# Kernel tuning notes

Measured on AMD Instinct MI355X. Metric: run time of the kernel, lower is better.

Reference implementation:

```python
import jax, jax.numpy as jnp
import numpy as np

N_NODES = 100000
EMB_DIM = 128
N_LAYERS = 3
N_EDGES = 1600000


def setup_inputs() -> dict:
    key = jax.random.key(0)
    ks = jax.random.split(key, 6)
    edge_index = jax.random.randint(ks[0], (2, N_EDGES), 0, N_NODES, dtype=jnp.int32)
    deg_inv = jax.random.uniform(ks[1], (N_NODES,), dtype=jnp.float32)
    node_emb = 0.02 * jax.random.normal(ks[2], (N_NODES, EMB_DIM), dtype=jnp.float32)
    W = jax.random.normal(ks[3], (N_LAYERS, EMB_DIM, EMB_DIM), dtype=jnp.float32) / np.sqrt(EMB_DIM)
    b = jnp.zeros((N_LAYERS, EMB_DIM), dtype=jnp.float32)
    gamma = jnp.ones((EMB_DIM,), dtype=jnp.float32)
    beta = jnp.zeros((EMB_DIM,), dtype=jnp.float32)
    return {"edge_index": edge_index, "deg_inv": deg_inv, "node_emb": node_emb,
            "W": W, "b": b, "gamma": gamma, "beta": beta}


def reference(edge_index, deg_inv, node_emb, W, b, gamma, beta):
    src, dst = edge_index[0], edge_index[1]
    x = node_emb  # [N, d]
    for l in range(N_LAYERS):
        # scatter-add neighbor aggregation: m[v] = sum_{(u->v)} x[u]
        m = jax.ops.segment_sum(x[src], dst, num_segments=N_NODES)  # [N, d]
        m = m * deg_inv[:, None]
        h = jax.nn.gelu(m @ W[l] + b[l], approximate=False)  # dropout=0 (eval)
        x = x + h  # residual
    # LayerNorm over feature dim
    mu = jnp.mean(x, axis=-1, keepdims=True)
    var = jnp.var(x, axis=-1, keepdims=True)
    x = (x - mu) * jax.lax.rsqrt(var + 1e-5) * gamma + beta
    return x
```

## Files before the change

kernel.cpp:

```cpp
#include <hip/hip_runtime.h>
#include <hip/hip_bf16.h>
#include <math.h>

#define N_NODES 100000
#define EMB 128
#define N_EDGES 1600000
#define N_LAYERS 3

#define NB 400
#define NPB 250
#define CAP 8192
#define CAPB 6144
#define BSTR 16
#define EPT 8
#define BUCKET_THREADS 512
#define BUCKET_BLOCKS ((N_EDGES + BUCKET_THREADS * EPT - 1) / (BUCKET_THREADS * EPT))

typedef __bf16 bf16x8 __attribute__((ext_vector_type(8)));
typedef float f32x4 __attribute__((ext_vector_type(4)));


__global__ __launch_bounds__(BUCKET_THREADS) void bucket_kernel(
    const int* __restrict__ src, const int* __restrict__ dst,
    int* __restrict__ bcur, unsigned* __restrict__ pairs) {
  __shared__ int scnt[NB];
  __shared__ int sbase[NB];
  const int t = threadIdx.x;
  if (t < NB) scnt[t] = 0;
  __syncthreads();
  unsigned pk[EPT];
  int bk[EPT], lofs[EPT];
  const int base_e = blockIdx.x * BUCKET_THREADS * EPT;
#pragma unroll
  for (int it = 0; it < EPT; ++it) {
    int i = base_e + it * BUCKET_THREADS + t;
    bk[it] = -1;
    if (i < N_EDGES) {
      int d = dst[i];
      int s = src[i];
      int b = d / NPB;
      int vloc = d - b * NPB;
      bk[it] = b;
      pk[it] = ((unsigned)vloc << 17) | (unsigned)s;
      lofs[it] = atomicAdd(&scnt[b], 1);
    }
  }
  __syncthreads();
  if (t < NB) sbase[t] = atomicAdd(&bcur[t * BSTR], scnt[t]);
  __syncthreads();
#pragma unroll
  for (int it = 0; it < EPT; ++it) {
    if (bk[it] >= 0) {
      int idx = sbase[bk[it]] + lofs[it];
      if (idx < CAP) pairs[(size_t)bk[it] * CAP + idx] = pk[it];
    }
  }
}

__device__ __forceinline__ int* scan512(int* pin, int* pout, int t) {
  for (int off = 1; off < 512; off <<= 1) {
    for (int i = t; i < 512; i += 256) {
      int v = pin[i];
      if (i >= off) v += pin[i - off];
      pout[i] = v;
    }
    __syncthreads();
    int* tmp = pin; pin = pout; pout = tmp;
  }
  return pin;
}

__global__ __launch_bounds__(256) void fillb_kernel(const unsigned* __restrict__ pairs,
                                                    const int* __restrict__ bcur,
                                                    int* __restrict__ row_ptr,
                                                    int* __restrict__ col) {
  __shared__ int sA[512], sB[512];
  __shared__ int cnt[NPB], cur[NPB];
  __shared__ unsigned pstage[CAPB];
  __shared__ int colstage[CAPB];
  const int t = threadIdx.x;
  const int b = blockIdx.x;

  for (int i = t; i < 512; i += 256) sA[i] = (i < NB) ? bcur[i * BSTR] : 0;
  __syncthreads();
  int* r = scan512(sA, sB, t);
  int base_b = b ? r[b - 1] : 0;
  int n = r[b] - base_b;
  if (n > CAP) n = CAP;
  const unsigned* pg = pairs + (size_t)b * CAP;
  const bool fits = (n <= CAPB);

  if (fits) for (int i = t; i < n; i += 256) pstage[i] = pg[i];
  if (t < NPB) cnt[t] = 0;
  __syncthreads();
  for (int i = t; i < n; i += 256) atomicAdd(&cnt[(fits ? pstage[i] : pg[i]) >> 17], 1);
  __syncthreads();
  for (int i = t; i < 512; i += 256) sA[i] = (i < NPB) ? cnt[i] : 0;
  __syncthreads();
  r = scan512(sA, sB, t);
  if (t < NPB) {
    int ex = r[t] - cnt[t];
    row_ptr[b * NPB + t] = base_b + ex;
    cur[t] = ex;
  }
  if (b == NB - 1 && t == 0) row_ptr[N_NODES] = N_EDGES;
  __syncthreads();
  for (int i = t; i < n; i += 256) {
    unsigned p = fits ? pstage[i] : pg[i];
    int pos = atomicAdd(&cur[p >> 17], 1);
    int s = (int)(p & 0x1FFFFu);
    if (fits) colstage[pos] = s;
    else col[base_b + pos] = s;
  }
  __syncthreads();
  if (fits) for (int i = t; i < n; i += 256) col[base_b + i] = colstage[i];
}


__global__ __launch_bounds__(256) void tobf16_kernel(const float* __restrict__ in,
                                                     __hip_bfloat16* __restrict__ xb) {
  size_t i = (size_t)blockIdx.x * 256 + threadIdx.x;
  const float4* p = (const float4*)in + i * 2;
  float4 a = p[0], b = p[1];
  union { __hip_bfloat16 h[8]; uint4 u; } r;
  r.h[0] = __float2bfloat16(a.x); r.h[1] = __float2bfloat16(a.y);
  r.h[2] = __float2bfloat16(a.z); r.h[3] = __float2bfloat16(a.w);
  r.h[4] = __float2bfloat16(b.x); r.h[5] = __float2bfloat16(b.y);
  r.h[6] = __float2bfloat16(b.z); r.h[7] = __float2bfloat16(b.w);
  ((uint4*)xb)[i] = r.u;
}

__global__ __launch_bounds__(256) void wt_kernel(const float* __restrict__ W,
                                                 __hip_bfloat16* __restrict__ WT) {
  int l = blockIdx.x;
  const float* Wl = W + (size_t)l * EMB * EMB;
  __hip_bfloat16* WTl = WT + (size_t)l * EMB * EMB;
  for (int i = threadIdx.x; i < EMB * EMB; i += 256) {
    int k = i >> 7, c = i & 127;
    WTl[c * EMB + k] = __float2bfloat16(Wl[i]);
  }
}


__device__ __forceinline__ float bf_lo(unsigned int w) { return __uint_as_float(w << 16); }
__device__ __forceinline__ float bf_hi(unsigned int w) { return __uint_as_float(w & 0xFFFF0000u); }

__device__ __forceinline__ float gelu_exact(float v) {
  return 0.5f * v * (1.f + erff(v * 0.70710678118654752f));
}

template <int LAST>
__global__ __launch_bounds__(256, LAST ? 5 : 8) void fused_kernel(
    const __hip_bfloat16* __restrict__ xb_in,
    const int* __restrict__ row_ptr,
    const int* __restrict__ col,
    const float* __restrict__ deg_inv,
    const __hip_bfloat16* __restrict__ WTl,
    const float* __restrict__ bias,
    __hip_bfloat16* __restrict__ xb_out,
    float* __restrict__ xf_out,
    const float* __restrict__ gamma,
    const float* __restrict__ beta) {
  __shared__ __hip_bfloat16 sM[32][136];
  __shared__ float sX[LAST ? 32 * 129 : 1];

  const int t = threadIdx.x;
  const int w = t >> 6;
  const int lane = t & 63;
  const int q = lane >> 4;
  const int l15 = lane & 15;
  const int row0b = blockIdx.x * 32;

  const char* gbase = (const char*)xb_in + l15 * 16;
  for (int nn = 0; nn < 8; ++nn) {
    const int v = __builtin_amdgcn_readfirstlane(row0b + w * 8 + nn);
    const int beg = row_ptr[v], end = row_ptr[v + 1];
    float a0 = 0.f, a1 = 0.f, a2 = 0.f, a3 = 0.f, a4 = 0.f, a5 = 0.f, a6 = 0.f, a7 = 0.f;
#define ACC8(W) { a0 += bf_lo(W.x); a1 += bf_hi(W.x); a2 += bf_lo(W.y); a3 += bf_hi(W.y); \
                  a4 += bf_lo(W.z); a5 += bf_hi(W.z); a6 += bf_lo(W.w); a7 += bf_hi(W.w); }
    int e = beg;
    for (; e + 16 <= end; e += 16) {
      int u0 = col[e + q];
      int u1 = col[e + 4 + q];
      int u2 = col[e + 8 + q];
      int u3 = col[e + 12 + q];
      uint4 w0 = *(const uint4*)(gbase + (size_t)u0 * 256);
      uint4 w1 = *(const uint4*)(gbase + (size_t)u1 * 256);
      uint4 w2 = *(const uint4*)(gbase + (size_t)u2 * 256);
      uint4 w3 = *(const uint4*)(gbase + (size_t)u3 * 256);
      ACC8(w0) ACC8(w1) ACC8(w2) ACC8(w3)
    }
    for (; e < end; e += 4) {
      int idx = e + q;
      bool valid = idx < end;
      int u = col[valid ? idx : beg];
      uint4 w0 = *(const uint4*)(gbase + (size_t)u * 256);
      if (valid) ACC8(w0)
    }
#undef ACC8
    a0 += __shfl_xor(a0, 16, 64); a0 += __shfl_xor(a0, 32, 64);
    a1 += __shfl_xor(a1, 16, 64); a1 += __shfl_xor(a1, 32, 64);
    a2 += __shfl_xor(a2, 16, 64); a2 += __shfl_xor(a2, 32, 64);
    a3 += __shfl_xor(a3, 16, 64); a3 += __shfl_xor(a3, 32, 64);
    a4 += __shfl_xor(a4, 16, 64); a4 += __shfl_xor(a4, 32, 64);
    a5 += __shfl_xor(a5, 16, 64); a5 += __shfl_xor(a5, 32, 64);
    a6 += __shfl_xor(a6, 16, 64); a6 += __shfl_xor(a6, 32, 64);
    a7 += __shfl_xor(a7, 16, 64); a7 += __shfl_xor(a7, 32, 64);
    if (q == 0) {
      float di = deg_inv[v];
      union { __hip_bfloat16 h[8]; uint4 u4; } r;
      r.h[0] = __float2bfloat16(a0 * di); r.h[1] = __float2bfloat16(a1 * di);
      r.h[2] = __float2bfloat16(a2 * di); r.h[3] = __float2bfloat16(a3 * di);
      r.h[4] = __float2bfloat16(a4 * di); r.h[5] = __float2bfloat16(a5 * di);
      r.h[6] = __float2bfloat16(a6 * di); r.h[7] = __float2bfloat16(a7 * di);
      *(uint4*)(&sM[w * 8 + nn][l15 * 8]) = r.u4;
    }
  }

  const int rh = w >> 1, ch = w & 1;
  const int lhi = q;
  bf16x8 bfr[4][4];
#pragma unroll
  for (int ct = 0; ct < 4; ++ct) {
    const __hip_bfloat16* wp = WTl + (size_t)(ch * 64 + ct * 16 + l15) * EMB + lhi * 8;
#pragma unroll
    for (int ks = 0; ks < 4; ++ks)
      bfr[ct][ks] = *(const bf16x8*)(wp + ks * 32);
  }
  __syncthreads();

  f32x4 acc[4];
#pragma unroll
  for (int ct = 0; ct < 4; ++ct) acc[ct] = (f32x4)(0.f);
#pragma unroll
  for (int ks = 0; ks < 4; ++ks) {
    bf16x8 af = *(const bf16x8*)(&sM[rh * 16 + l15][lhi * 8 + ks * 32]);
#pragma unroll
    for (int ct = 0; ct < 4; ++ct)
      acc[ct] = __builtin_amdgcn_mfma_f32_16x16x32_bf16(af, bfr[ct][ks], acc[ct], 0, 0, 0);
  }

#pragma unroll
  for (int ct = 0; ct < 4; ++ct) {
    const int colg = ch * 64 + ct * 16 + l15;
    const float bb = bias[colg];
#pragma unroll
    for (int j = 0; j < 4; ++j) {
      const int rloc = rh * 16 + lhi * 4 + j;
      const size_t off = (size_t)(row0b + rloc) * EMB + colg;
      float xv = __bfloat162float(xb_in[off]) + gelu_exact(acc[ct][j] + bb);
      if (!LAST) xb_out[off] = __float2bfloat16(xv);
      else sX[rloc * 129 + colg] = xv;
    }
  }

  if (LAST) {
    __syncthreads();
    float g1 = gamma[lane], g2 = gamma[lane + 64];
    float b1 = beta[lane], b2 = beta[lane + 64];
    for (int rr = 0; rr < 8; ++rr) {
      int r = w * 8 + rr;
      float v1 = sX[r * 129 + lane], v2 = sX[r * 129 + lane + 64];
      float s = v1 + v2;
      float sq = fmaf(v1, v1, v2 * v2);
      for (int off = 1; off < 64; off <<= 1) {
        s += __shfl_xor(s, off, 64);
        sq += __shfl_xor(sq, off, 64);
      }
      float mu = s * (1.f / EMB);
      float var = sq * (1.f / EMB) - mu * mu;
      float rstd = rsqrtf(var + 1e-5f);
      size_t rowoff = (size_t)(row0b + r) * EMB;
      xf_out[rowoff + lane] = (v1 - mu) * rstd * g1 + b1;
      xf_out[rowoff + lane + 64] = (v2 - mu) * rstd * g2 + b2;
    }
  }
}


extern "C" void kernel_launch(void* const* d_in, const int* in_sizes, int n_in,
                              void* d_out, int out_size, void* d_ws, size_t ws_size,
                              hipStream_t stream) {
  const int* edge_index = (const int*)d_in[0];
  const float* deg_inv = (const float*)d_in[1];
  const float* node_emb = (const float*)d_in[2];
  const float* W = (const float*)d_in[3];
  const float* b = (const float*)d_in[4];
  const float* gamma = (const float*)d_in[5];
  const float* beta = (const float*)d_in[6];
  const int* src = edge_index;
  const int* dst = edge_index + N_EDGES;
  float* x = (float*)d_out;

  char* ws = (char*)d_ws;
  auto take = [&](size_t bytes) {
    char* p = ws;
    ws += (bytes + 255) & ~(size_t)255;
    return p;
  };
  __hip_bfloat16* xbA = (__hip_bfloat16*)take((size_t)N_NODES * EMB * 2);
  __hip_bfloat16* xbB = (__hip_bfloat16*)take((size_t)N_NODES * EMB * 2);
  __hip_bfloat16* WT = (__hip_bfloat16*)take((size_t)N_LAYERS * EMB * EMB * 2);
  int* row_ptr = (int*)take((N_NODES + 1) * sizeof(int));
  int* col = (int*)take(N_EDGES * sizeof(int));
  int* bcur = (int*)take(NB * BSTR * sizeof(int));
  unsigned* pairs = (unsigned*)xbB;

  hipMemsetAsync(bcur, 0, NB * BSTR * sizeof(int), stream);

  tobf16_kernel<<<N_NODES * EMB / 8 / 256, 256, 0, stream>>>(node_emb, xbA);
  wt_kernel<<<N_LAYERS, 256, 0, stream>>>(W, WT);

  bucket_kernel<<<BUCKET_BLOCKS, BUCKET_THREADS, 0, stream>>>(src, dst, bcur, pairs);
  fillb_kernel<<<NB, 256, 0, stream>>>(pairs, bcur, row_ptr, col);

  const int NBLK = N_NODES / 32;
  fused_kernel<0><<<NBLK, 256, 0, stream>>>(xbA, row_ptr, col, deg_inv,
                                            WT, b, xbB, nullptr, nullptr, nullptr);
  fused_kernel<0><<<NBLK, 256, 0, stream>>>(xbB, row_ptr, col, deg_inv,
                                            WT + (size_t)EMB * EMB, b + EMB,
                                            xbA, nullptr, nullptr, nullptr);
  fused_kernel<1><<<NBLK, 256, 0, stream>>>(xbA, row_ptr, col, deg_inv,
                                            WT + (size_t)2 * EMB * EMB, b + 2 * EMB,
                                            nullptr, x, gamma, beta);
}
```

Before: 353.9 us.

## Use 1024-thread blocks with two nodes per wave and one MFMA column tile each

The fused layer kernel moves from 256-thread blocks (4 waves, 8 nodes each) to 1024-thread blocks (16 waves, 2 nodes each). The 32x128 MFMA product is split so each wave computes one 16x16 output tile, and the LayerNorm epilogue is remapped to match. The aim is to shorten each wave's serial chain of neighbor gathers and expose more independent memory traffic per block. The risks are larger blocks being harder to schedule and a strict launch bound that may force register limits or spills.

After: 315.7 us. 10.8% less time.

```diff
diff --git a/kernel.cpp b/kernel.cpp
--- a/kernel.cpp
+++ b/kernel.cpp
@@ -150,7 +150,7 @@
 }
 
 template <int LAST>
-__global__ __launch_bounds__(256, LAST ? 5 : 8) void fused_kernel(
+__global__ __launch_bounds__(1024, 8) void fused_kernel(
     const __hip_bfloat16* __restrict__ xb_in,
     const int* __restrict__ row_ptr,
     const int* __restrict__ col,
@@ -172,8 +172,8 @@
   const int row0b = blockIdx.x * 32;
 
   const char* gbase = (const char*)xb_in + l15 * 16;
-  for (int nn = 0; nn < 8; ++nn) {
-    const int v = __builtin_amdgcn_readfirstlane(row0b + w * 8 + nn);
+  for (int nn = 0; nn < 2; ++nn) {
+    const int v = __builtin_amdgcn_readfirstlane(row0b + w * 2 + nn);
     const int beg = row_ptr[v], end = row_ptr[v + 1];
     float a0 = 0.f, a1 = 0.f, a2 = 0.f, a3 = 0.f, a4 = 0.f, a5 = 0.f, a6 = 0.f, a7 = 0.f;
 #define ACC8(W) { a0 += bf_lo(W.x); a1 += bf_hi(W.x); a2 += bf_lo(W.y); a3 += bf_hi(W.y); \
@@ -213,42 +213,36 @@
       r.h[2] = __float2bfloat16(a2 * di); r.h[3] = __float2bfloat16(a3 * di);
       r.h[4] = __float2bfloat16(a4 * di); r.h[5] = __float2bfloat16(a5 * di);
       r.h[6] = __float2bfloat16(a6 * di); r.h[7] = __float2bfloat16(a7 * di);
-      *(uint4*)(&sM[w * 8 + nn][l15 * 8]) = r.u4;
-    }
-  }
-
-  const int rh = w >> 1, ch = w & 1;
-  const int lhi = q;
-  bf16x8 bfr[4][4];
-#pragma unroll
-  for (int ct = 0; ct < 4; ++ct) {
-    const __hip_bfloat16* wp = WTl + (size_t)(ch * 64 + ct * 16 + l15) * EMB + lhi * 8;
+      *(uint4*)(&sM[w * 2 + nn][l15 * 8]) = r.u4;
+    }
+  }
+
+  const int rh = w >> 3;
+  const int ct8 = w & 7;
+  bf16x8 bfr[4];
+  {
+    const __hip_bfloat16* wp = WTl + (size_t)(ct8 * 16 + l15) * EMB + q * 8;
 #pragma unroll
     for (int ks = 0; ks < 4; ++ks)
-      bfr[ct][ks] = *(const bf16x8*)(wp + ks * 32);
-  }
-  __syncthreads();
-
-  f32x4 acc[4];
-#pragma unroll
-  for (int ct = 0; ct < 4; ++ct) acc[ct] = (f32x4)(0.f);
+      bfr[ks] = *(const bf16x8*)(wp + ks * 32);
+  }
+  __syncthreads();
+
+  f32x4 acc = (f32x4)(0.f);
 #pragma unroll
   for (int ks = 0; ks < 4; ++ks) {
-    bf16x8 af = *(const bf16x8*)(&sM[rh * 16 + l15][lhi * 8 + ks * 32]);
-#pragma unroll
-    for (int ct = 0; ct < 4; ++ct)
-      acc[ct] = __builtin_amdgcn_mfma_f32_16x16x32_bf16(af, bfr[ct][ks], acc[ct], 0, 0, 0);
-  }
-
-#pragma unroll
-  for (int ct = 0; ct < 4; ++ct) {
-    const int colg = ch * 64 + ct * 16 + l15;
+    bf16x8 af = *(const bf16x8*)(&sM[rh * 16 + l15][q * 8 + ks * 32]);
+    acc = __builtin_amdgcn_mfma_f32_16x16x32_bf16(af, bfr[ks], acc, 0, 0, 0);
+  }
+
+  {
+    const int colg = ct8 * 16 + l15;
     const float bb = bias[colg];
 #pragma unroll
     for (int j = 0; j < 4; ++j) {
-      const int rloc = rh * 16 + lhi * 4 + j;
+      const int rloc = rh * 16 + q * 4 + j;
       const size_t off = (size_t)(row0b + rloc) * EMB + colg;
-      float xv = __bfloat162float(xb_in[off]) + gelu_exact(acc[ct][j] + bb);
+      float xv = __bfloat162float(xb_in[off]) + gelu_exact(acc[j] + bb);
       if (!LAST) xb_out[off] = __float2bfloat16(xv);
       else sX[rloc * 129 + colg] = xv;
     }
@@ -258,8 +252,8 @@
     __syncthreads();
     float g1 = gamma[lane], g2 = gamma[lane + 64];
     float b1 = beta[lane], b2 = beta[lane + 64];
-    for (int rr = 0; rr < 8; ++rr) {
-      int r = w * 8 + rr;
+    for (int rr = 0; rr < 2; ++rr) {
+      int r = w * 2 + rr;
       float v1 = sX[r * 129 + lane], v2 = sX[r * 129 + lane + 64];
       float s = v1 + v2;
       float sq = fmaf(v1, v1, v2 * v2);
@@ -315,12 +309,12 @@
   fillb_kernel<<<NB, 256, 0, stream>>>(pairs, bcur, row_ptr, col);
 
   const int NBLK = N_NODES / 32;
-  fused_kernel<0><<<NBLK, 256, 0, stream>>>(xbA, row_ptr, col, deg_inv,
-                                            WT, b, xbB, nullptr, nullptr, nullptr);
-  fused_kernel<0><<<NBLK, 256, 0, stream>>>(xbB, row_ptr, col, deg_inv,
-                                            WT + (size_t)EMB * EMB, b + EMB,
-                                            xbA, nullptr, nullptr, nullptr);
-  fused_kernel<1><<<NBLK, 256, 0, stream>>>(xbA, row_ptr, col, deg_inv,
-                                            WT + (size_t)2 * EMB * EMB, b + 2 * EMB,
-                                            nullptr, x, gamma, beta);
-}
+  fused_kernel<0><<<NBLK, 1024, 0, stream>>>(xbA, row_ptr, col, deg_inv,
+                                             WT, b, xbB, nullptr, nullptr, nullptr);
+  fused_kernel<0><<<NBLK, 1024, 0, stream>>>(xbB, row_ptr, col, deg_inv,
+                                             WT + (size_t)EMB * EMB, b + EMB,
+                                             xbA, nullptr, nullptr, nullptr);
+  fused_kernel<1><<<NBLK, 1024, 0, stream>>>(xbA, row_ptr, col, deg_inv,
+                                             WT + (size_t)2 * EMB * EMB, b + 2 * EMB,
+                                             nullptr, x, gamma, beta);
+}
```
